# Optimization experiments

Measured on AMD Instinct MI355X. Metric: run time of the kernel, lower is better.

## Reference

```python
import jax, jax.numpy as jnp
import numpy as np

SL, BS, D, H = 2048, 4, 512, 8
NH = D // H  # per-head dim (nhid)
SCALE = np.float32(1.0 / np.sqrt(NH))


def setup_inputs() -> dict:
    key = jax.random.key(0)
    ks = jax.random.split(key, 8)
    s = np.float32(0.02)
    return {
        "input_tensor": jax.random.normal(ks[0], (SL, BS, D), jnp.float32),
        "keys_vector": jax.random.normal(ks[1], (SL, BS, D), jnp.float32),
        "values_vector": jax.random.normal(ks[2], (SL, BS, D), jnp.float32),
        # learned projections: query/keys/values -> num_heads*nhid, plus output proj
        "Wq": jax.random.normal(ks[3], (D, D), jnp.float32) * s,
        "bq": jnp.zeros((D,), jnp.float32),
        "Wk": jax.random.normal(ks[4], (D, D), jnp.float32) * s,
        "bk": jnp.zeros((D,), jnp.float32),
        "Wv": jax.random.normal(ks[5], (D, D), jnp.float32) * s,
        "bv": jnp.zeros((D,), jnp.float32),
        "Wo": jax.random.normal(ks[6], (D, D), jnp.float32) * s,
        "bo": jnp.zeros((D,), jnp.float32),
    }


def reference(input_tensor, keys_vector, values_vector, Wq, bq, Wk, bk, Wv, bv, Wo, bo):
    # Vectorized equivalent of the per-step Python loop with incremental mask
    # (mask=True): query step i attends to keys 0..i -> causal attention.
    q = (input_tensor @ Wq + bq).reshape(SL, BS, H, NH)   # [q,b,h,n]
    k = (keys_vector @ Wk + bk).reshape(SL, BS, H, NH)    # [s,b,h,n]
    v = (values_vector @ Wv + bv).reshape(SL, BS, H, NH)  # [s,b,h,n]
    scores = jnp.einsum('qbhn,sbhn->qsbh', q, k) * SCALE  # [q,s,b,h]
    causal = jnp.tril(jnp.ones((SL, SL), dtype=bool))     # allow s <= q
    scores = jnp.where(causal[:, :, None, None], scores, jnp.float32(-1e9))
    w = jax.nn.softmax(scores, axis=1)                    # softmax over keys s
    out = jnp.einsum('qsbh,sbhn->qbhn', w, v).reshape(SL, BS, D)
    return out @ Wo + bo                                  # [q,b,D]
```

## Files before the change

kernel.cpp:

```cpp
#include <hip/hip_runtime.h>

typedef __attribute__((ext_vector_type(8))) short short8;
typedef __attribute__((ext_vector_type(4))) short short4v;
typedef __attribute__((ext_vector_type(4))) float f32x4;
typedef __attribute__((ext_vector_type(2))) unsigned int uint2v;

constexpr int SL = 2048, BS = 4, D = 512, H = 8, NH = 64;
constexpr int M_ROWS = SL * BS;
constexpr float SCALE = 0.125f;
constexpr float LOG2E = 1.44269504088896340736f;

__device__ __forceinline__ unsigned short f2bf(float f) {
  union { float f; unsigned u; } v; v.f = f;
  unsigned r = v.u + 0x7FFFu + ((v.u >> 16) & 1u);
  return (unsigned short)(r >> 16);
}

__device__ __forceinline__ unsigned cvt_pk_bf16(float a, float b) {
  unsigned r;
  asm("v_cvt_pk_bf16_f32 %0, %1, %2" : "=v"(r) : "v"(a), "v"(b));
  return r;
}

__device__ __forceinline__ float fast_exp2(float x) {
  float r;
  asm("v_exp_f32 %0, %1" : "=v"(r) : "v"(x));
  return r;
}

__device__ __forceinline__ void gl16(const void* g, void* l) {
  __builtin_amdgcn_global_load_lds(
      (const __attribute__((address_space(1))) unsigned int*)g,
      (__attribute__((address_space(3))) unsigned int*)l, 16, 0, 0);
}

__global__ __launch_bounds__(256) void prep_wt(
    const float* __restrict__ w0, const float* __restrict__ w1,
    const float* __restrict__ w2, const float* __restrict__ w3,
    unsigned short* __restrict__ wtb) {
  __shared__ float tl[64][65];
  const int tid = threadIdx.x;
  const int wi = blockIdx.x >> 6, t6 = blockIdx.x & 63;
  const int k0 = (t6 >> 3) * 64, n0 = (t6 & 7) * 64;
  const float* W = wi == 0 ? w0 : (wi == 1 ? w1 : (wi == 2 ? w2 : w3));
  unsigned short* WT = wtb + (size_t)wi * D * D;

#pragma unroll
  for (int i = 0; i < 4; ++i) {
    int k = (tid >> 4) + i * 16, n4 = (tid & 15) * 4;
    f32x4 v = *reinterpret_cast<const f32x4*>(&W[(size_t)(k0 + k) * D + n0 + n4]);
#pragma unroll
    for (int j = 0; j < 4; ++j) tl[n4 + j][k] = v[j];
  }
  __syncthreads();
#pragma unroll
  for (int i = 0; i < 2; ++i) {
    int n = (tid >> 3) + i * 32, k8 = (tid & 7) * 8;
    union { unsigned u[4]; short8 s; } pk;
#pragma unroll
    for (int j = 0; j < 4; ++j)
      pk.u[j] = cvt_pk_bf16(tl[n][k8 + 2 * j], tl[n][k8 + 2 * j + 1]);
    *reinterpret_cast<short8*>(&WT[(size_t)(n0 + n) * D + k0 + k8]) = pk.s;
  }
}

template <bool A_BF16, int OUT_MODE>
__device__ __forceinline__ void gemm_bt_body(const void* __restrict__ Ap,
                                             const unsigned short* __restrict__ BT,
                                             const float* __restrict__ bias,
                                             void* __restrict__ Outp, float scale,
                                             unsigned short* smem) {
  const int tid = threadIdx.x;
  const int brow = blockIdx.x * 128;
  const int bcol = blockIdx.y * 128;
  const int lane = tid & 63;
  const int wid = tid >> 6;
  const int wr = (wid >> 1) * 64;
  const int wc = (wid & 1) * 64;
  const int r = lane & 15;
  const int g = lane >> 4;

  auto a_buf = [&](int b) { return smem + b * 16384; };
  auto b_buf = [&](int b) { return smem + b * 16384 + 8192; };

  f32x4 acc[4][4];
#pragma unroll
  for (int m = 0; m < 4; ++m)
#pragma unroll
    for (int n = 0; n < 4; ++n) acc[m][n] = f32x4{0.f, 0.f, 0.f, 0.f};

  auto STAGE_B = [&](int kt, int bsel) {
    unsigned short* bl = b_buf(bsel);
#pragma unroll
    for (int j = 0; j < 4; ++j) {
      int c = j * 256 + tid;
      int row = c >> 3, c8 = (c & 7) ^ (row & 7);
      gl16(&BT[(size_t)(bcol + row) * D + kt + c8 * 8], &bl[c * 8]);
    }
  };
  auto STAGE_A_LDS = [&](int kt, int bsel) {
    const unsigned short* A = (const unsigned short*)Ap;
    unsigned short* al = a_buf(bsel);
#pragma unroll
    for (int j = 0; j < 4; ++j) {
      int c = j * 256 + tid;
      int row = c >> 3, c8 = (c & 7) ^ (row & 7);
      gl16(&A[(size_t)(brow + row) * D + kt + c8 * 8], &al[c * 8]);
    }
  };
  auto A_LOAD = [&](int kt, f32x4 (&va)[4][2]) {
    const float* A = (const float*)Ap;
#pragma unroll
    for (int j = 0; j < 4; ++j) {
      int c = j * 256 + tid;
      int row = c >> 3, c8 = (c & 7) ^ (row & 7);
      const float* ap = &A[(size_t)(brow + row) * D + kt + c8 * 8];
      va[j][0] = *reinterpret_cast<const f32x4*>(ap);
      va[j][1] = *reinterpret_cast<const f32x4*>(ap + 4);
    }
  };
  auto A_WRITE = [&](f32x4 (&va)[4][2], int bsel) {
    unsigned short* al = a_buf(bsel);
#pragma unroll
    for (int j = 0; j < 4; ++j) {
      int c = j * 256 + tid;
      union { unsigned u[4]; short8 s; } pk;
      pk.u[0] = cvt_pk_bf16(va[j][0][0], va[j][0][1]);
      pk.u[1] = cvt_pk_bf16(va[j][0][2], va[j][0][3]);
      pk.u[2] = cvt_pk_bf16(va[j][1][0], va[j][1][1]);
      pk.u[3] = cvt_pk_bf16(va[j][1][2], va[j][1][3]);
      *reinterpret_cast<short8*>(&al[c * 8]) = pk.s;
    }
  };
  auto COMPUTE = [&](int bsel) {
    const unsigned short* al = a_buf(bsel);
    const unsigned short* bl = b_buf(bsel);
#pragma unroll
    for (int kk2 = 0; kk2 < 2; ++kk2) {
      short8 af[4], bfr[4];
#pragma unroll
      for (int m = 0; m < 4; ++m)
        af[m] = *reinterpret_cast<const short8*>(
            &al[(wr + m * 16 + r) * 64 + (((kk2 * 4 + g) ^ (r & 7)) * 8)]);
#pragma unroll
      for (int n = 0; n < 4; ++n)
        bfr[n] = *reinterpret_cast<const short8*>(
            &bl[(wc + n * 16 + r) * 64 + (((kk2 * 4 + g) ^ (r & 7)) * 8)]);
      __builtin_amdgcn_s_setprio(1);
#pragma unroll
      for (int m = 0; m < 4; ++m)
#pragma unroll
        for (int n = 0; n < 4; ++n)
          acc[m][n] = __builtin_amdgcn_mfma_f32_16x16x32_bf16(af[m], bfr[n], acc[m][n], 0, 0, 0);
      __builtin_amdgcn_s_setprio(0);
    }
  };

  if (A_BF16) {
    STAGE_A_LDS(0, 0);
    STAGE_B(0, 0);
    asm volatile("s_waitcnt vmcnt(0)" ::: "memory");
  } else {
    f32x4 va[4][2];
    A_LOAD(0, va);
    STAGE_B(0, 0);
    asm volatile("s_waitcnt vmcnt(4)" ::: "memory");
    A_WRITE(va, 0);
    asm volatile("s_waitcnt vmcnt(0) lgkmcnt(0)" ::: "memory");
  }
  __builtin_amdgcn_s_barrier();

#pragma unroll
  for (int t = 0; t < 8; ++t) {
    const int cur = t & 1, nxt = cur ^ 1;
    const int ktn = (t + 1) * 64;
    __builtin_amdgcn_sched_barrier(0);
    f32x4 va[4][2];
    if (t < 7) {
      if (A_BF16) {
        STAGE_A_LDS(ktn, nxt);
        STAGE_B(ktn, nxt);
      } else {
        A_LOAD(ktn, va);
        STAGE_B(ktn, nxt);
      }
    }
    __builtin_amdgcn_sched_barrier(0);
    COMPUTE(cur);
    if (t < 7) {
      if (!A_BF16) {
        asm volatile("s_waitcnt vmcnt(4)" ::: "memory");
        A_WRITE(va, nxt);
      }
      asm volatile("s_waitcnt vmcnt(0) lgkmcnt(0)" ::: "memory");
      __builtin_amdgcn_s_barrier();
    }
  }

  if (OUT_MODE == 2) {
    unsigned short* sc = smem;
    const int wr4 = wr >> 2;
#pragma unroll
    for (int m = 0; m < 4; ++m)
#pragma unroll
      for (int n = 0; n < 4; ++n) {
        int col = wc + n * 16 + r;
        float bv = bias[bcol + col];
        int sl = wr4 + m * 4 + g;
        int pp = ((sl >> 2) & 3) * 8 + ((sl >> 4) & 1) * 4 + (sl & 3);
#pragma unroll
        for (int rr = 0; rr < 4; ++rr) {
          int c = (rr * 4 + (pp >> 3)) ^ (col & 7);
          sc[col * 128 + c * 8 + (pp & 7)] = f2bf((acc[m][n][rr] + bv) * scale);
        }
      }
    asm volatile("s_waitcnt lgkmcnt(0)" ::: "memory");
    __builtin_amdgcn_s_barrier();
    unsigned short* VT = (unsigned short*)Outp;
#pragma unroll
    for (int i2 = 0; i2 < 2; ++i2) {
      int q = tid * 2 + i2;
      int col = q >> 2, bb = q & 3;
      int gcol = bcol + col, hh = gcol >> 6, nh = gcol & 63;
      size_t gbase = (((size_t)bb * H + hh) * NH + nh) * SL + (brow >> 2);
#pragma unroll
      for (int j = 0; j < 4; ++j) {
        short8 v = *reinterpret_cast<const short8*>(
            &sc[col * 128 + (((bb * 4 + j) ^ (col & 7)) * 8)]);
        *reinterpret_cast<short8*>(&VT[gbase + j * 8]) = v;
      }
    }
  } else {
#pragma unroll
    for (int m = 0; m < 4; ++m)
#pragma unroll
      for (int n = 0; n < 4; ++n) {
        int gcol = bcol + wc + n * 16 + r;
        float bv = bias[gcol];
#pragma unroll
        for (int rr = 0; rr < 4; ++rr) {
          int grow = brow + wr + m * 16 + g * 4 + rr;
          float val = (acc[m][n][rr] + bv) * scale;
          if (OUT_MODE == 0)
            ((float*)Outp)[(size_t)grow * D + gcol] = val;
          else
            ((unsigned short*)Outp)[(size_t)grow * D + gcol] = f2bf(val);
        }
      }
  }
}

__global__ __launch_bounds__(256, 2) void qkv_gemm(
    const float* __restrict__ x0, const float* __restrict__ x1, const float* __restrict__ x2,
    const unsigned short* __restrict__ wtb,
    const float* __restrict__ b0, const float* __restrict__ b1, const float* __restrict__ b2,
    unsigned short* __restrict__ q_out, unsigned short* __restrict__ k_out,
    unsigned short* __restrict__ vt_out) {
  __shared__ __align__(16) unsigned short smem[2 * 16384];
  int z = blockIdx.z;
  const float* X = z == 0 ? x0 : (z == 1 ? x1 : x2);
  const unsigned short* WT = wtb + (size_t)z * D * D;
  const float* B = z == 0 ? b0 : (z == 1 ? b1 : b2);
  float scale = (z == 0) ? SCALE * LOG2E : 1.0f;
  if (z == 2)
    gemm_bt_body<false, 2>(X, WT, B, vt_out, scale, smem);
  else
    gemm_bt_body<false, 1>(X, WT, B, z == 0 ? q_out : k_out, scale, smem);
}

__global__ __launch_bounds__(256, 2) void gemm_oproj(
    const unsigned short* __restrict__ A, const unsigned short* __restrict__ WT,
    const float* __restrict__ B, float* __restrict__ Outp) {
  __shared__ __align__(16) unsigned short smem[2 * 16384];
  gemm_bt_body<true, 0>(A, WT, B, Outp, 1.0f, smem);
}

__global__ __launch_bounds__(256, 3) void flash_attn(
    const unsigned short* __restrict__ Q, const unsigned short* __restrict__ K,
    const unsigned short* __restrict__ Vt, unsigned short* __restrict__ O) {
  __shared__ __align__(16) unsigned short k_lds[3][64 * 64];
  __shared__ __align__(16) unsigned short v_lds[3][64 * 64];

  const int bid = blockIdx.x;
  const int s = bid >> 5, idx = bid & 31;
  const int grp = idx & 7;
  const int bh = grp * 4 + (idx >> 3);
  const int b = bh >> 3, h = bh & 7;
  const int qt = (s < 8) ? 31 - s : (s < 16) ? s + 8 : (s < 24) ? 31 - s : s - 24;
  const int q0 = qt * 64;

  const int tid = threadIdx.x;
  const int w = tid >> 6, lane = tid & 63;
  const int r = lane & 15, g = lane >> 4;
  const int swz = (r & 7) << 3;

  const unsigned short* Qb = Q + (size_t)b * D + h * NH;
  const unsigned short* Kb = K + (size_t)b * D + h * NH;
  const unsigned short* Vb = Vt + ((size_t)(b * H + h) * NH) * SL;
  unsigned short* Ob = O + (size_t)b * D + h * NH;

  auto STAGE = [&](int kt, int bsel) {
    unsigned short* kl = &k_lds[bsel][0];
    unsigned short* vl = &v_lds[bsel][0];
#pragma unroll
    for (int j = 0; j < 2; ++j) {
      int c = j * 256 + tid;
      int row = c >> 3, c8 = (c & 7) ^ (row & 7);
      gl16(&Kb[(size_t)(kt * 64 + row) * (BS * D) + c8 * 8], &kl[c * 8]);
      gl16(&Vb[(size_t)row * SL + kt * 64 + c8 * 8], &vl[c * 8]);
    }
  };

  STAGE(0, 0);
  if (qt >= 1) STAGE(1, 1);

  short8 qf[2];
#pragma unroll
  for (int kk = 0; kk < 2; ++kk)
    qf[kk] = *reinterpret_cast<const short8*>(
        &Qb[(size_t)(q0 + w * 16 + r) * (BS * D) + kk * 32 + g * 8]);

  f32x4 oa[4];
#pragma unroll
  for (int n = 0; n < 4; ++n) oa[n] = f32x4{0.f, 0.f, 0.f, 0.f};
  float mr = -1e30f, lrp = 0.f;

  int bsel = 0;
  for (int kt = 0; kt <= qt; ++kt) {
    if (kt < qt)
      asm volatile("s_waitcnt vmcnt(8)" ::: "memory");
    else
      asm volatile("s_waitcnt vmcnt(0)" ::: "memory");
    __builtin_amdgcn_s_barrier();
    __builtin_amdgcn_sched_barrier(0);
    if (kt + 2 <= qt) {
      int nb = bsel + 2; if (nb >= 3) nb -= 3;
      STAGE(kt + 2, nb);
    }

    const unsigned short* kl = &k_lds[bsel][0];
    const unsigned short* vl = &v_lds[bsel][0];
    short8 kf[2][4];
#pragma unroll
    for (int kk = 0; kk < 2; ++kk)
#pragma unroll
      for (int n = 0; n < 4; ++n)
        kf[kk][n] = *reinterpret_cast<const short8*>(
            &kl[(n * 16 + r) * 64 + ((kk * 32 + g * 8) ^ swz)]);

    f32x4 sv[4];
#pragma unroll
    for (int n = 0; n < 4; ++n) sv[n] = f32x4{0.f, 0.f, 0.f, 0.f};
#pragma unroll
    for (int kk = 0; kk < 2; ++kk)
#pragma unroll
      for (int n = 0; n < 4; ++n)
        sv[n] = __builtin_amdgcn_mfma_f32_16x16x32_bf16(kf[kk][n], qf[kk], sv[n], 0, 0, 0);

    short8 vt[2][4];
#pragma unroll
    for (int kk = 0; kk < 2; ++kk)
#pragma unroll
      for (int n = 0; n < 4; ++n)
        vt[kk][n] = *reinterpret_cast<const short8*>(
            &vl[(n * 16 + r) * 64 + ((kk * 32 + g * 8) ^ swz)]);

    if (kt == qt) {
      int qrow = q0 + w * 16 + r;
#pragma unroll
      for (int n = 0; n < 4; ++n)
#pragma unroll
        for (int rr = 0; rr < 4; ++rr)
          if (kt * 64 + n * 16 + g * 4 + rr > qrow) sv[n][rr] = -1e30f;
    }

    float t0 = fmaxf(fmaxf(sv[0][0], sv[0][1]), sv[0][2]);
    float t1 = fmaxf(fmaxf(sv[0][3], sv[1][0]), sv[1][1]);
    float t2 = fmaxf(fmaxf(sv[1][2], sv[1][3]), sv[2][0]);
    float t3 = fmaxf(fmaxf(sv[2][1], sv[2][2]), sv[2][3]);
    float t4 = fmaxf(fmaxf(sv[3][0], sv[3][1]), sv[3][2]);
    float mxl = fmaxf(fmaxf(fmaxf(t0, t1), fmaxf(t2, t3)), fmaxf(t4, sv[3][3]));
    bool need = __any(mxl > mr + 8.f);
    float mold = mr;
    float mnew = mold;
    if (need) {
      float mx = fmaxf(mxl, __shfl_xor(mxl, 16));
      mx = fmaxf(mx, __shfl_xor(mx, 32));
      mnew = fmaxf(mold, mx);
    }
#pragma unroll
    for (int n = 0; n < 4; ++n)
#pragma unroll
      for (int rr = 0; rr < 4; ++rr)
        sv[n][rr] = fast_exp2(sv[n][rr] - mnew);
    float a0 = (sv[0][0] + sv[0][1]) + (sv[0][2] + sv[0][3]);
    float a1 = (sv[1][0] + sv[1][1]) + (sv[1][2] + sv[1][3]);
    float a2 = (sv[2][0] + sv[2][1]) + (sv[2][2] + sv[2][3]);
    float a3 = (sv[3][0] + sv[3][1]) + (sv[3][2] + sv[3][3]);
    float psl = (a0 + a1) + (a2 + a3);
    if (need) {
      float sf = fast_exp2(mold - mnew);
      mr = mnew;
      lrp = lrp * sf + psl;
#pragma unroll
      for (int n = 0; n < 4; ++n) oa[n] *= sf;
    } else {
      lrp += psl;
    }

    short8 pf[2];
#pragma unroll
    for (int kk = 0; kk < 2; ++kk) {
      union { unsigned u[4]; short8 s8; } P;
      P.u[0] = cvt_pk_bf16(sv[2 * kk][0], sv[2 * kk][1]);
      P.u[1] = cvt_pk_bf16(sv[2 * kk][2], sv[2 * kk][3]);
      P.u[2] = cvt_pk_bf16(sv[2 * kk + 1][0], sv[2 * kk + 1][1]);
      P.u[3] = cvt_pk_bf16(sv[2 * kk + 1][2], sv[2 * kk + 1][3]);
      pf[kk] = P.s8;
    }

#pragma unroll
    for (int kk = 0; kk < 2; ++kk)
#pragma unroll
      for (int n = 0; n < 4; ++n)
        oa[n] = __builtin_amdgcn_mfma_f32_16x16x32_bf16(vt[kk][n], pf[kk], oa[n], 0, 0, 0);

    ++bsel; if (bsel >= 3) bsel = 0;
  }

  __syncthreads();
  {
    unsigned short* pw = &k_lds[0][0] + w * 2048;
    float lr = lrp + __shfl_xor(lrp, 16);
    lr += __shfl_xor(lr, 32);
    float inv = 1.0f / lr;
#pragma unroll
    for (int n = 0; n < 4; ++n) {
      uint2v pk;
      pk.x = cvt_pk_bf16(oa[n][0] * inv, oa[n][1] * inv);
      pk.y = cvt_pk_bf16(oa[n][2] * inv, oa[n][3] * inv);
      *reinterpret_cast<uint2v*>(&pw[r * 64 + ((n * 16 + g * 4) ^ swz)]) = pk;
    }
    asm volatile("s_waitcnt lgkmcnt(0)" ::: "memory");
    __builtin_amdgcn_sched_barrier(0);
#pragma unroll
    for (int i2 = 0; i2 < 2; ++i2) {
      int c = i2 * 64 + lane;
      int row = c >> 3, c8 = c & 7;
      short8 v = *reinterpret_cast<const short8*>(&pw[row * 64 + c8 * 8]);
      *reinterpret_cast<short8*>(
          &Ob[(size_t)(q0 + w * 16 + row) * (BS * D) + ((c8 ^ (row & 7)) * 8)]) = v;
    }
  }
}

extern "C" void kernel_launch(void* const* d_in, const int* in_sizes, int n_in,
                              void* d_out, int out_size, void* d_ws, size_t ws_size,
                              hipStream_t stream) {
  const float* x  = (const float*)d_in[0];
  const float* kx = (const float*)d_in[1];
  const float* vx = (const float*)d_in[2];
  const float* Wq = (const float*)d_in[3];
  const float* bq = (const float*)d_in[4];
  const float* Wk = (const float*)d_in[5];
  const float* bk = (const float*)d_in[6];
  const float* Wv = (const float*)d_in[7];
  const float* bv = (const float*)d_in[8];
  const float* Wo = (const float*)d_in[9];
  const float* bo = (const float*)d_in[10];

  unsigned short* ws = (unsigned short*)d_ws;
  unsigned short* qb  = ws;
  unsigned short* kb  = ws + (size_t)M_ROWS * D;
  unsigned short* vtb = ws + (size_t)M_ROWS * D * 2;
  unsigned short* wtb = ws + (size_t)M_ROWS * D * 3;

  prep_wt<<<dim3(256), dim3(256), 0, stream>>>(Wq, Wk, Wv, Wo, wtb);
  qkv_gemm<<<dim3(64, 4, 3), dim3(256), 0, stream>>>(x, kx, vx, wtb, bq, bk, bv,
                                                     qb, kb, vtb);
  flash_attn<<<dim3(1024), dim3(256), 0, stream>>>(qb, kb, vtb, qb);
  gemm_oproj<<<dim3(64, 4, 1), dim3(256), 0, stream>>>(qb, wtb + (size_t)3 * D * D,
                                                       bo, (float*)d_out);
}
```

Baseline: 77.03 us.

## Load GEMM A operand directly into registers instead of staging through LDS

The shared GEMM body now has each wave load its own A-operand fragments straight from global memory into registers, converting fp32 to bf16 in registers. Only the B tile is staged in LDS, which halves LDS use and removes the A LDS writes and reads and their barrier dependency. The cost is that A rows are no longer shared across the two column waves, so A is read twice from global or L2. It also adds register pressure from the double-buffered fp32 A values, which may hurt occupancy at two blocks per CU.

```diff
diff --git a/kernel.cpp b/kernel.cpp
--- a/kernel.cpp
+++ b/kernel.cpp
@@ -80,8 +80,7 @@
   const int r = lane & 15;
   const int g = lane >> 4;
 
-  auto a_buf = [&](int b) { return smem + b * 16384; };
-  auto b_buf = [&](int b) { return smem + b * 16384 + 8192; };
+  auto b_buf = [&](int b) { return smem + b * 8192; };
 
   f32x4 acc[4][4];
 #pragma unroll
@@ -98,106 +97,111 @@
       gl16(&BT[(size_t)(bcol + row) * D + kt + c8 * 8], &bl[c * 8]);
     }
   };
-  auto STAGE_A_LDS = [&](int kt, int bsel) {
+
+  const float* arowf[4];
+  const unsigned short* arowh[4];
+  if (A_BF16) {
     const unsigned short* A = (const unsigned short*)Ap;
-    unsigned short* al = a_buf(bsel);
-#pragma unroll
-    for (int j = 0; j < 4; ++j) {
-      int c = j * 256 + tid;
-      int row = c >> 3, c8 = (c & 7) ^ (row & 7);
-      gl16(&A[(size_t)(brow + row) * D + kt + c8 * 8], &al[c * 8]);
-    }
+#pragma unroll
+    for (int m = 0; m < 4; ++m)
+      arowh[m] = &A[(size_t)(brow + wr + m * 16 + r) * D + g * 8];
+  } else {
+    const float* A = (const float*)Ap;
+#pragma unroll
+    for (int m = 0; m < 4; ++m)
+      arowf[m] = &A[(size_t)(brow + wr + m * 16 + r) * D + g * 8];
+  }
+
+  f32x4 va[4][2][2];
+  short8 va8[2][4][2];
+
+  auto A_LOAD_F32 = [&](int kt) {
+#pragma unroll
+    for (int m = 0; m < 4; ++m)
+#pragma unroll
+      for (int kk = 0; kk < 2; ++kk) {
+        const float* p = arowf[m] + kt + kk * 32;
+        va[m][kk][0] = *reinterpret_cast<const f32x4*>(p);
+        va[m][kk][1] = *reinterpret_cast<const f32x4*>(p + 4);
+      }
   };
-  auto A_LOAD = [&](int kt, f32x4 (&va)[4][2]) {
-    const float* A = (const float*)Ap;
-#pragma unroll
-    for (int j = 0; j < 4; ++j) {
-      int c = j * 256 + tid;
-      int row = c >> 3, c8 = (c & 7) ^ (row & 7);
-      const float* ap = &A[(size_t)(brow + row) * D + kt + c8 * 8];
-      va[j][0] = *reinterpret_cast<const f32x4*>(ap);
-      va[j][1] = *reinterpret_cast<const f32x4*>(ap + 4);
-    }
+  auto A_LOAD_BF16 = [&](int kt, int buf) {
+#pragma unroll
+    for (int m = 0; m < 4; ++m)
+#pragma unroll
+      for (int kk = 0; kk < 2; ++kk)
+        va8[buf][m][kk] = *reinterpret_cast<const short8*>(arowh[m] + kt + kk * 32);
   };
-  auto A_WRITE = [&](f32x4 (&va)[4][2], int bsel) {
-    unsigned short* al = a_buf(bsel);
-#pragma unroll
-    for (int j = 0; j < 4; ++j) {
-      int c = j * 256 + tid;
-      union { unsigned u[4]; short8 s; } pk;
-      pk.u[0] = cvt_pk_bf16(va[j][0][0], va[j][0][1]);
-      pk.u[1] = cvt_pk_bf16(va[j][0][2], va[j][0][3]);
-      pk.u[2] = cvt_pk_bf16(va[j][1][0], va[j][1][1]);
-      pk.u[3] = cvt_pk_bf16(va[j][1][2], va[j][1][3]);
-      *reinterpret_cast<short8*>(&al[c * 8]) = pk.s;
-    }
-  };
-  auto COMPUTE = [&](int bsel) {
-    const unsigned short* al = a_buf(bsel);
-    const unsigned short* bl = b_buf(bsel);
-#pragma unroll
-    for (int kk2 = 0; kk2 < 2; ++kk2) {
-      short8 af[4], bfr[4];
-#pragma unroll
-      for (int m = 0; m < 4; ++m)
-        af[m] = *reinterpret_cast<const short8*>(
-            &al[(wr + m * 16 + r) * 64 + (((kk2 * 4 + g) ^ (r & 7)) * 8)]);
-#pragma unroll
-      for (int n = 0; n < 4; ++n)
-        bfr[n] = *reinterpret_cast<const short8*>(
-            &bl[(wc + n * 16 + r) * 64 + (((kk2 * 4 + g) ^ (r & 7)) * 8)]);
-      __builtin_amdgcn_s_setprio(1);
-#pragma unroll
-      for (int m = 0; m < 4; ++m)
-#pragma unroll
-        for (int n = 0; n < 4; ++n)
-          acc[m][n] = __builtin_amdgcn_mfma_f32_16x16x32_bf16(af[m], bfr[n], acc[m][n], 0, 0, 0);
-      __builtin_amdgcn_s_setprio(0);
-    }
-  };
-
-  if (A_BF16) {
-    STAGE_A_LDS(0, 0);
-    STAGE_B(0, 0);
-    asm volatile("s_waitcnt vmcnt(0)" ::: "memory");
-  } else {
-    f32x4 va[4][2];
-    A_LOAD(0, va);
-    STAGE_B(0, 0);
-    asm volatile("s_waitcnt vmcnt(4)" ::: "memory");
-    A_WRITE(va, 0);
-    asm volatile("s_waitcnt vmcnt(0) lgkmcnt(0)" ::: "memory");
-  }
+
+  STAGE_B(0, 0);
+  if (A_BF16) A_LOAD_BF16(0, 0); else A_LOAD_F32(0);
+  if (A_BF16)
+    asm volatile("s_waitcnt vmcnt(8)" ::: "memory");
+  else
+    asm volatile("s_waitcnt vmcnt(16)" ::: "memory");
   __builtin_amdgcn_s_barrier();
+  __builtin_amdgcn_sched_barrier(0);
 
 #pragma unroll
   for (int t = 0; t < 8; ++t) {
     const int cur = t & 1, nxt = cur ^ 1;
     const int ktn = (t + 1) * 64;
+
+    short8 af[4][2];
+    if (A_BF16) {
+#pragma unroll
+      for (int m = 0; m < 4; ++m)
+#pragma unroll
+        for (int kk = 0; kk < 2; ++kk) af[m][kk] = va8[cur][m][kk];
+    } else {
+#pragma unroll
+      for (int m = 0; m < 4; ++m)
+#pragma unroll
+        for (int kk = 0; kk < 2; ++kk) {
+          union { unsigned u[4]; short8 s; } pk;
+          pk.u[0] = cvt_pk_bf16(va[m][kk][0][0], va[m][kk][0][1]);
+          pk.u[1] = cvt_pk_bf16(va[m][kk][0][2], va[m][kk][0][3]);
+          pk.u[2] = cvt_pk_bf16(va[m][kk][1][0], va[m][kk][1][1]);
+          pk.u[3] = cvt_pk_bf16(va[m][kk][1][2], va[m][kk][1][3]);
+          af[m][kk] = pk.s;
+        }
+    }
+
+    if (t < 7) {
+      STAGE_B(ktn, nxt);
+      if (A_BF16) A_LOAD_BF16(ktn, nxt); else A_LOAD_F32(ktn);
+    }
     __builtin_amdgcn_sched_barrier(0);
-    f32x4 va[4][2];
+
+    const unsigned short* bl = b_buf(cur);
+#pragma unroll
+    for (int kk = 0; kk < 2; ++kk) {
+      short8 bfr[4];
+#pragma unroll
+      for (int n = 0; n < 4; ++n)
+        bfr[n] = *reinterpret_cast<const short8*>(
+            &bl[(wc + n * 16 + r) * 64 + (((kk * 4 + g) ^ (r & 7)) * 8)]);
+      __builtin_amdgcn_s_setprio(1);
+#pragma unroll
+      for (int m = 0; m < 4; ++m)
+#pragma unroll
+        for (int n = 0; n < 4; ++n)
+          acc[m][n] = __builtin_amdgcn_mfma_f32_16x16x32_bf16(af[m][kk], bfr[n], acc[m][n], 0, 0, 0);
+      __builtin_amdgcn_s_setprio(0);
+    }
+
     if (t < 7) {
-      if (A_BF16) {
-        STAGE_A_LDS(ktn, nxt);
-        STAGE_B(ktn, nxt);
-      } else {
-        A_LOAD(ktn, va);
-        STAGE_B(ktn, nxt);
-      }
-    }
-    __builtin_amdgcn_sched_barrier(0);
-    COMPUTE(cur);
-    if (t < 7) {
-      if (!A_BF16) {
-        asm volatile("s_waitcnt vmcnt(4)" ::: "memory");
-        A_WRITE(va, nxt);
-      }
-      asm volatile("s_waitcnt vmcnt(0) lgkmcnt(0)" ::: "memory");
+      if (A_BF16)
+        asm volatile("s_waitcnt vmcnt(8)" ::: "memory");
+      else
+        asm volatile("s_waitcnt vmcnt(16)" ::: "memory");
       __builtin_amdgcn_s_barrier();
+      __builtin_amdgcn_sched_barrier(0);
     }
   }
 
   if (OUT_MODE == 2) {
+    __syncthreads();
     unsigned short* sc = smem;
     const int wr4 = wr >> 2;
 #pragma unroll
@@ -256,7 +260,7 @@
     const float* __restrict__ b0, const float* __restrict__ b1, const float* __restrict__ b2,
     unsigned short* __restrict__ q_out, unsigned short* __restrict__ k_out,
     unsigned short* __restrict__ vt_out) {
-  __shared__ __align__(16) unsigned short smem[2 * 16384];
+  __shared__ __align__(16) unsigned short smem[2 * 8192];
   int z = blockIdx.z;
   const float* X = z == 0 ? x0 : (z == 1 ? x1 : x2);
   const unsigned short* WT = wtb + (size_t)z * D * D;
@@ -271,7 +275,7 @@
 __global__ __launch_bounds__(256, 2) void gemm_oproj(
     const unsigned short* __restrict__ A, const unsigned short* __restrict__ WT,
     const float* __restrict__ B, float* __restrict__ Outp) {
-  __shared__ __align__(16) unsigned short smem[2 * 16384];
+  __shared__ __align__(16) unsigned short smem[2 * 8192];
   gemm_bt_body<true, 0>(A, WT, B, Outp, 1.0f, smem);
 }
 
```

New measurement: 111.4 us. 44.6% more time.

## Single-buffer A tile in GEMMs, prefetch A to registers, raise occupancy

Applied to the files above, without the earlier changes.

The GEMM body now keeps one A tile in LDS instead of two and double-buffers only B. A fragments are read into registers before a barrier, and the next A tile is written into the same buffer. For the fp32-input QKV GEMM, A is prefetched two stages ahead in registers. This cuts LDS use from 64KB to 48KB per block so launch bounds can rise to 3 blocks per CU. The cost is an extra barrier per iteration and more live registers, which may limit the intended occupancy.

```diff
diff --git a/kernel.cpp b/kernel.cpp
--- a/kernel.cpp
+++ b/kernel.cpp
@@ -80,8 +80,8 @@
   const int r = lane & 15;
   const int g = lane >> 4;
 
-  auto a_buf = [&](int b) { return smem + b * 16384; };
-  auto b_buf = [&](int b) { return smem + b * 16384 + 8192; };
+  unsigned short* a_lds = smem;
+  auto b_buf = [&](int b) { return smem + 8192 + b * 8192; };
 
   f32x4 acc[4][4];
 #pragma unroll
@@ -98,14 +98,13 @@
       gl16(&BT[(size_t)(bcol + row) * D + kt + c8 * 8], &bl[c * 8]);
     }
   };
-  auto STAGE_A_LDS = [&](int kt, int bsel) {
+  auto STAGE_A_LDS = [&](int kt) {
     const unsigned short* A = (const unsigned short*)Ap;
-    unsigned short* al = a_buf(bsel);
 #pragma unroll
     for (int j = 0; j < 4; ++j) {
       int c = j * 256 + tid;
       int row = c >> 3, c8 = (c & 7) ^ (row & 7);
-      gl16(&A[(size_t)(brow + row) * D + kt + c8 * 8], &al[c * 8]);
+      gl16(&A[(size_t)(brow + row) * D + kt + c8 * 8], &a_lds[c * 8]);
     }
   };
   auto A_LOAD = [&](int kt, f32x4 (&va)[4][2]) {
@@ -119,8 +118,7 @@
       va[j][1] = *reinterpret_cast<const f32x4*>(ap + 4);
     }
   };
-  auto A_WRITE = [&](f32x4 (&va)[4][2], int bsel) {
-    unsigned short* al = a_buf(bsel);
+  auto A_WRITE = [&](f32x4 (&va)[4][2]) {
 #pragma unroll
     for (int j = 0; j < 4; ++j) {
       int c = j * 256 + tid;
@@ -129,75 +127,91 @@
       pk.u[1] = cvt_pk_bf16(va[j][0][2], va[j][0][3]);
       pk.u[2] = cvt_pk_bf16(va[j][1][0], va[j][1][1]);
       pk.u[3] = cvt_pk_bf16(va[j][1][2], va[j][1][3]);
-      *reinterpret_cast<short8*>(&al[c * 8]) = pk.s;
+      *reinterpret_cast<short8*>(&a_lds[c * 8]) = pk.s;
     }
   };
-  auto COMPUTE = [&](int bsel) {
-    const unsigned short* al = a_buf(bsel);
-    const unsigned short* bl = b_buf(bsel);
-#pragma unroll
-    for (int kk2 = 0; kk2 < 2; ++kk2) {
-      short8 af[4], bfr[4];
-#pragma unroll
-      for (int m = 0; m < 4; ++m)
-        af[m] = *reinterpret_cast<const short8*>(
-            &al[(wr + m * 16 + r) * 64 + (((kk2 * 4 + g) ^ (r & 7)) * 8)]);
-#pragma unroll
-      for (int n = 0; n < 4; ++n)
-        bfr[n] = *reinterpret_cast<const short8*>(
-            &bl[(wc + n * 16 + r) * 64 + (((kk2 * 4 + g) ^ (r & 7)) * 8)]);
-      __builtin_amdgcn_s_setprio(1);
-#pragma unroll
-      for (int m = 0; m < 4; ++m)
-#pragma unroll
-        for (int n = 0; n < 4; ++n)
-          acc[m][n] = __builtin_amdgcn_mfma_f32_16x16x32_bf16(af[m], bfr[n], acc[m][n], 0, 0, 0);
-      __builtin_amdgcn_s_setprio(0);
-    }
-  };
+
+  f32x4 va[4][2];
 
   if (A_BF16) {
-    STAGE_A_LDS(0, 0);
+    STAGE_A_LDS(0);
     STAGE_B(0, 0);
     asm volatile("s_waitcnt vmcnt(0)" ::: "memory");
   } else {
-    f32x4 va[4][2];
     A_LOAD(0, va);
     STAGE_B(0, 0);
     asm volatile("s_waitcnt vmcnt(4)" ::: "memory");
-    A_WRITE(va, 0);
-    asm volatile("s_waitcnt vmcnt(0) lgkmcnt(0)" ::: "memory");
+    A_WRITE(va);
+    A_LOAD(64, va);
+    asm volatile("s_waitcnt vmcnt(8)" ::: "memory");
+    asm volatile("s_waitcnt lgkmcnt(0)" ::: "memory");
   }
   __builtin_amdgcn_s_barrier();
+  __builtin_amdgcn_sched_barrier(0);
 
 #pragma unroll
   for (int t = 0; t < 8; ++t) {
     const int cur = t & 1, nxt = cur ^ 1;
     const int ktn = (t + 1) * 64;
+
+    if (t < 7) STAGE_B(ktn, nxt);
+
+    short8 af[4][2];
+#pragma unroll
+    for (int kk = 0; kk < 2; ++kk)
+#pragma unroll
+      for (int m = 0; m < 4; ++m)
+        af[m][kk] = *reinterpret_cast<const short8*>(
+            &a_lds[(wr + m * 16 + r) * 64 + (((kk * 4 + g) ^ (r & 7)) * 8)]);
+    asm volatile("s_waitcnt lgkmcnt(0)" ::: "memory");
     __builtin_amdgcn_sched_barrier(0);
-    f32x4 va[4][2];
+    __builtin_amdgcn_s_barrier();
+    __builtin_amdgcn_sched_barrier(0);
+
     if (t < 7) {
       if (A_BF16) {
-        STAGE_A_LDS(ktn, nxt);
-        STAGE_B(ktn, nxt);
+        STAGE_A_LDS(ktn);
       } else {
-        A_LOAD(ktn, va);
-        STAGE_B(ktn, nxt);
+        asm volatile("s_waitcnt vmcnt(4)" ::: "memory");
+        A_WRITE(va);
+        if (t < 6) A_LOAD(ktn + 64, va);
       }
     }
     __builtin_amdgcn_sched_barrier(0);
-    COMPUTE(cur);
+
+    const unsigned short* bl = b_buf(cur);
+#pragma unroll
+    for (int kk = 0; kk < 2; ++kk) {
+      short8 bfr[4];
+#pragma unroll
+      for (int n = 0; n < 4; ++n)
+        bfr[n] = *reinterpret_cast<const short8*>(
+            &bl[(wc + n * 16 + r) * 64 + (((kk * 4 + g) ^ (r & 7)) * 8)]);
+      __builtin_amdgcn_s_setprio(1);
+#pragma unroll
+      for (int m = 0; m < 4; ++m)
+#pragma unroll
+        for (int n = 0; n < 4; ++n)
+          acc[m][n] = __builtin_amdgcn_mfma_f32_16x16x32_bf16(af[m][kk], bfr[n], acc[m][n], 0, 0, 0);
+      __builtin_amdgcn_s_setprio(0);
+    }
+
     if (t < 7) {
-      if (!A_BF16) {
-        asm volatile("s_waitcnt vmcnt(4)" ::: "memory");
-        A_WRITE(va, nxt);
+      if (A_BF16) {
+        asm volatile("s_waitcnt vmcnt(0)" ::: "memory");
+      } else if (t < 6) {
+        asm volatile("s_waitcnt vmcnt(8)" ::: "memory");
+      } else {
+        asm volatile("s_waitcnt vmcnt(0)" ::: "memory");
       }
-      asm volatile("s_waitcnt vmcnt(0) lgkmcnt(0)" ::: "memory");
+      asm volatile("s_waitcnt lgkmcnt(0)" ::: "memory");
       __builtin_amdgcn_s_barrier();
+      __builtin_amdgcn_sched_barrier(0);
     }
   }
 
   if (OUT_MODE == 2) {
+    __syncthreads();
     unsigned short* sc = smem;
     const int wr4 = wr >> 2;
 #pragma unroll
@@ -250,13 +264,13 @@
   }
 }
 
-__global__ __launch_bounds__(256, 2) void qkv_gemm(
+__global__ __launch_bounds__(256, 3) void qkv_gemm(
     const float* __restrict__ x0, const float* __restrict__ x1, const float* __restrict__ x2,
     const unsigned short* __restrict__ wtb,
     const float* __restrict__ b0, const float* __restrict__ b1, const float* __restrict__ b2,
     unsigned short* __restrict__ q_out, unsigned short* __restrict__ k_out,
     unsigned short* __restrict__ vt_out) {
-  __shared__ __align__(16) unsigned short smem[2 * 16384];
+  __shared__ __align__(16) unsigned short smem[3 * 8192];
   int z = blockIdx.z;
   const float* X = z == 0 ? x0 : (z == 1 ? x1 : x2);
   const unsigned short* WT = wtb + (size_t)z * D * D;
@@ -268,10 +282,10 @@
     gemm_bt_body<false, 1>(X, WT, B, z == 0 ? q_out : k_out, scale, smem);
 }
 
-__global__ __launch_bounds__(256, 2) void gemm_oproj(
+__global__ __launch_bounds__(256, 3) void gemm_oproj(
     const unsigned short* __restrict__ A, const unsigned short* __restrict__ WT,
     const float* __restrict__ B, float* __restrict__ Outp) {
-  __shared__ __align__(16) unsigned short smem[2 * 16384];
+  __shared__ __align__(16) unsigned short smem[3 * 8192];
   gemm_bt_body<true, 0>(A, WT, B, Outp, 1.0f, smem);
 }
 
```

After: 82.09 us. +6.6%, slower.
